# Kernel tuning notes

Measured on AMD Instinct MI355X. Metric: run time of the kernel, lower is better.

## Reference

```python
import jax, jax.numpy as jnp
import numpy as np

L = 768          # temporal feature length
C_IN = 2048      # feature channels
NA = 10          # anchor scales per position
NC = 21          # num classes (20 + bg)
PRE_NMS = 1024   # pre-NMS top-k
POST_NMS = 128   # fixed proposal count after NMS
NMS_THR = 0.7
SCALE = 1.0      # cfg.Process.new_dilation*new_cluster/Frame
ANCHOR_SIZES = np.array([2., 4., 5., 6., 8., 9., 10., 12., 14., 16.], np.float32)


def _conv(x, w, b, pad=0):
    # x: [N,C,T], w: [O,I,K]
    y = jax.lax.conv_general_dilated(x, w, (1,), [(pad, pad)],
                                     dimension_numbers=('NCH', 'OIH', 'NCH'))
    return y + b[None, :, None]


def _lin(x, w, b):
    return x @ w.T + b


def _forward(feature, p):
    f = _conv(feature, p['w1f'], p['b1f'], 1)
    f = _conv(f, p['w2f'], p['b2f'], 1)
    x = _conv(f, p['wc1'], p['bc1'], 0)                      # [1,512,L]
    # SegmentProposal tower (relu only after conv4, as in source)
    h = _conv(x, p['sp1w'], p['sp1b'], 1)
    h = _conv(h, p['sp2w'], p['sp2b'], 1)
    h = _conv(h, p['sp3w'], p['sp3b'], 1)
    h = jax.nn.relu(_conv(h, p['sp4w'], p['sp4b'], 1))
    cls_score = _conv(h, p['spcw'], p['spcb'], 0)            # [1,2*NA,L]
    seg_pred = _conv(h, p['spsw'], p['spsb'], 0)             # [1,2*NA,L]

    def _resh(t):  # [1,2NA,L] -> [L*NA,2]  (transpose(2,1).view(B,L,C/2,2))
        return jnp.transpose(t, (0, 2, 1)).reshape(-1, 2)

    cls2 = _resh(cls_score)
    cls_prob = jax.nn.softmax(cls2, -1)
    off2 = _resh(seg_pred)

    # anchors: (center, half_len) per position per scale, position-major
    centers = (jnp.arange(L, dtype=jnp.float32) + 0.5) * SCALE
    halves = jnp.asarray(ANCHOR_SIZES) * 0.5
    a_c = jnp.repeat(centers, NA)
    a_h = jnp.tile(halves, L)
    im_info = L * SCALE

    # apply offsets: center shift + log-length scale, clip to video extent
    c = a_c + off2[:, 0] * (2.0 * a_h)
    hl = a_h * jnp.exp(off2[:, 1])
    s = jnp.clip(c - hl, 0.0, im_info)
    e = jnp.clip(c + hl, 0.0, im_info)
    scores = cls_prob[:, 1]

    top_sc, top_i = jax.lax.top_k(scores, PRE_NMS)
    ss, ee = s[top_i], e[top_i]

    def body(i, keep):
        inter = jnp.maximum(0., jnp.minimum(ee, ee[i]) - jnp.maximum(ss, ss[i]))
        union = (ee - ss) + (ee[i] - ss[i]) - inter
        iou = inter / jnp.maximum(union, 1e-8)
        sup = (iou > NMS_THR) & (jnp.arange(PRE_NMS) > i) & keep[i]
        return keep & ~sup

    keep = jax.lax.fori_loop(0, PRE_NMS, body, jnp.ones(PRE_NMS, bool))
    order = jnp.argsort((~keep).astype(jnp.int32), stable=True)  # kept first, score order
    sel = order[:POST_NMS]
    pidx = top_i[sel]
    ps, pe = s[pidx], e[pidx]
    pbbox = jnp.stack([(ps + pe) * 0.5, (pe - ps) * 0.5], -1)    # (center, half)

    # map proposals to feature index range (floor/ceil + clamp, as in source)
    st = jnp.clip(jnp.floor((pbbox[:, 0] - pbbox[:, 1]) / SCALE), 0, L - 1).astype(jnp.int32)
    en = jnp.clip(jnp.ceil((pbbox[:, 0] + pbbox[:, 1]) / SCALE), 0, L - 1).astype(jnp.int32)
    en = jnp.maximum(en, st)

    feat = f[0]                                              # [C_IN, L]
    tpos = jnp.arange(L)
    bins = jnp.arange(7)

    def roi_pool(se):  # AdaptiveMaxPool1d(7) over feat[:, s0:e0+1]
        s0, e0 = se
        ln = e0 - s0 + 1
        bs = s0 + (bins * ln) // 7
        be = s0 + ((bins + 1) * ln + 6) // 7 - 1
        m = (tpos[None, :] >= bs[:, None]) & (tpos[None, :] <= be[:, None])  # [7,L]
        v = jnp.where(m[None], feat[:, None, :], -jnp.inf)   # [C_IN,7,L]
        return v.max(-1)                                     # [C_IN,7]

    spp = jax.lax.map(roi_pool, (st, en))                    # [K,C_IN,7]

    y = _conv(spp, p['wc2'], p['bc2'], 0)
    y = _conv(y, p['w3'], p['b3'], 1)
    y = jax.nn.relu(_conv(y, p['w4'], p['b4'], 1))
    y = _conv(y, p['w5'], p['b5'], 1)
    y = jax.nn.relu(_conv(y, p['w6'], p['b6'], 1))
    y = y.reshape(y.shape[0], -1)                            # [K, 512*7]
    y = _lin(y, p['fc1w'], p['fc1b'])
    # Relation attention is computed but unused in the source forward -> omitted
    y = jax.nn.relu(y)
    y = _lin(y, p['fc2w'], p['fc2b'])
    y = _lin(y, p['fc3w'], p['fc3b'])
    obj_cls = _lin(y, p['clsw'], p['clsb'])                  # [K,NC]
    obj_off = _lin(y, p['boxw'], p['boxb']).reshape(-1, NC - 1, 2)
    cls_sel = cls2[pidx]                                     # [K,2]
    off_sel = off2[pidx]                                     # [K,2]
    return cls_sel, off_sel, obj_cls, obj_off


_PARAM_SHAPES = {
    'w1f': (2048, 2048, 3), 'b1f': (2048,),
    'w2f': (2048, 2048, 3), 'b2f': (2048,),
    'wc1': (512, 2048, 1), 'bc1': (512,),
    'sp1w': (512, 512, 3), 'sp1b': (512,),
    'sp2w': (512, 512, 3), 'sp2b': (512,),
    'sp3w': (512, 512, 3), 'sp3b': (512,),
    'sp4w': (512, 512, 3), 'sp4b': (512,),
    'spcw': (2 * NA, 512, 1), 'spcb': (2 * NA,),
    'spsw': (2 * NA, 512, 1), 'spsb': (2 * NA,),
    'wc2': (512, 2048, 1), 'bc2': (512,),
    'w3': (512, 512, 3), 'b3': (512,),
    'w4': (512, 512, 3), 'b4': (512,),
    'w5': (512, 512, 3), 'b5': (512,),
    'w6': (512, 512, 3), 'b6': (512,),
    'fc1w': (512, 512 * 7), 'fc1b': (512,),
    'fc2w': (256, 512), 'fc2b': (256,),
    'fc3w': (128, 256), 'fc3b': (128,),
    'clsw': (NC, 128), 'clsb': (NC,),
    'boxw': (2 * (NC - 1), 128), 'boxb': (2 * (NC - 1),),
}


def setup_inputs() -> dict:
    key = jax.random.key(0)
    inp = {'feature': jax.random.normal(jax.random.fold_in(key, 0), (1, C_IN, L), jnp.float32)}
    for i, (name, shp) in enumerate(sorted(_PARAM_SHAPES.items())):
        k = jax.random.fold_in(key, i + 1)
        inp[name] = jax.random.normal(k, shp, jnp.float32) * 0.02
    return inp


def reference(feature, b1f, b2f, b3, b4, b5, b6, bc1, bc2, boxb, boxw, clsb, clsw,
              fc1b, fc1w, fc2b, fc2w, fc3b, fc3w, sp1b, sp1w, sp2b, sp2w, sp3b, sp3w,
              sp4b, sp4w, spcb, spcw, spsb, spsw, w1f, w2f, w3, w4, w5, w6,
              wc1, wc2):
    p = dict(w1f=w1f, b1f=b1f, w2f=w2f, b2f=b2f, wc1=wc1, bc1=bc1,
             sp1w=sp1w, sp1b=sp1b, sp2w=sp2w, sp2b=sp2b, sp3w=sp3w, sp3b=sp3b,
             sp4w=sp4w, sp4b=sp4b, spcw=spcw, spcb=spcb, spsw=spsw, spsb=spsb,
             wc2=wc2, bc2=bc2, w3=w3, b3=b3, w4=w4, b4=b4, w5=w5, b5=b5,
             w6=w6, b6=b6, fc1w=fc1w, fc1b=fc1b, fc2w=fc2w, fc2b=fc2b,
             fc3w=fc3w, fc3b=fc3b, clsw=clsw, clsb=clsb, boxw=boxw, boxb=boxb)
    return _forward(feature, p)
```

## Files before the change

### kernel.cpp

```cpp
#include <hip/hip_runtime.h>

typedef __attribute__((ext_vector_type(8))) short short8;
typedef __attribute__((ext_vector_type(4))) float float4v;

__device__ __forceinline__ float bf(unsigned short u) {
    return __uint_as_float(((unsigned int)u) << 16);
}
__device__ __forceinline__ unsigned short f2b(float f) {
    unsigned int u = __float_as_uint(f);
    unsigned int r = (u + 0x7FFFu + ((u >> 16) & 1u)) >> 16;
    return (unsigned short)r;
}

__constant__ float c_anchors[10] = {2.f,4.f,5.f,6.f,8.f,9.f,10.f,12.f,14.f,16.f};

__global__ __launch_bounds__(256) void zeroXt_kernel(unsigned short* __restrict__ Xt, int CI) {
    int i = blockIdx.x * 256 + threadIdx.x;
    if (i < 2 * CI) {
        int row = (i >= CI) ? 769 : 0;
        int co = (i >= CI) ? (i - CI) : i;
        Xt[(size_t)row * CI + co] = 0;
        Xt[(size_t)770 * CI + (size_t)row * CI + co] = 0;
    }
}

__global__ __launch_bounds__(256) void decomp_kernel(const float* __restrict__ src,
                                                     unsigned short* __restrict__ Xt, int CI) {
    __shared__ float T[32][33];
    int l0 = blockIdx.x * 32, ci0 = blockIdx.y * 32;
    int tid = threadIdx.x;
#pragma unroll
    for (int i = 0; i < 4; i++) {
        int slot = tid + 256 * i;
        int r = slot >> 5, c = slot & 31;
        T[r][c] = src[(size_t)(ci0 + r) * 768 + l0 + c];
    }
    __syncthreads();
    unsigned short* Xh = Xt;
    unsigned short* Xl = Xt + (size_t)770 * CI;
#pragma unroll
    for (int i = 0; i < 4; i++) {
        int slot = tid + 256 * i;
        int li = slot >> 5, cc = slot & 31;
        float v = T[cc][li];
        unsigned short h = f2b(v);
        float lo = v - bf(h);
        size_t o = (size_t)(l0 + li + 1) * CI + ci0 + cc;
        Xh[o] = h;
        Xl[o] = f2b(lo);
    }
}

template <int TAPS>
__global__ __launch_bounds__(512, 6) void convmm_kernel(const float* __restrict__ W,
                                                        const unsigned short* __restrict__ Xt,
                                                        float* __restrict__ G,
                                                        int CO, int CI, int S) {
    constexpr int RS = TAPS * 32 + 8;
    __shared__ unsigned short At[2][64 * RS];
    __shared__ unsigned short Bt[2][130 * 40];
    int tid = threadIdx.x;
    int lane = tid & 63, wid = tid >> 6;
    int q = lane >> 4, ln = lane & 15;
    int co0 = blockIdx.x * 64;
    int l0 = blockIdx.y * 128;
    int s = blockIdx.z;
    int kPer = CI / S, cis = s * kPer;
    const unsigned short* Xh = Xt;
    const unsigned short* Xl = Xt + (size_t)770 * CI;

    float4v zero4 = {0.f, 0.f, 0.f, 0.f};
    float4v acc[2][2];
    acc[0][0] = zero4; acc[0][1] = zero4; acc[1][0] = zero4; acc[1][1] = zero4;

    int wave_m = (wid >> 2) * 32;
    int wave_n = (wid & 3) * 32;

    for (int kb = 0; kb < kPer; kb += 32) {
        int cib = cis + kb;
        if (TAPS == 3) {
#pragma unroll
            for (int i = 0; i < 2; i++) {
                int slot = tid + 512 * i;
                int row = slot >> 4, ci0 = (slot & 15) * 2;
                const float* wp = W + ((size_t)(co0 + row) * CI + cib + ci0) * 3;
                float fa[6];
#pragma unroll
                for (int j = 0; j < 6; j++) fa[j] = wp[j];
#pragma unroll
                for (int t = 0; t < 3; t++) {
                    unsigned short h0 = f2b(fa[t]);
                    unsigned short h1 = f2b(fa[t + 3]);
                    unsigned short e0 = f2b(fa[t] - bf(h0));
                    unsigned short e1 = f2b(fa[t + 3] - bf(h1));
                    *(unsigned int*)&At[0][row * RS + t * 32 + ci0] =
                        (unsigned int)h0 | ((unsigned int)h1 << 16);
                    *(unsigned int*)&At[1][row * RS + t * 32 + ci0] =
                        (unsigned int)e0 | ((unsigned int)e1 << 16);
                }
            }
        } else {
            int row = tid >> 3, ci0 = (tid & 7) * 4;
            float4 wv = *(const float4*)(W + (size_t)(co0 + row) * CI + cib + ci0);
            float fa[4] = {wv.x, wv.y, wv.z, wv.w};
            unsigned short h[4], e[4];
#pragma unroll
            for (int j = 0; j < 4; j++) {
                h[j] = f2b(fa[j]);
                e[j] = f2b(fa[j] - bf(h[j]));
            }
            unsigned long long hp = (unsigned long long)h[0] | ((unsigned long long)h[1] << 16) |
                                    ((unsigned long long)h[2] << 32) | ((unsigned long long)h[3] << 48);
            unsigned long long ep = (unsigned long long)e[0] | ((unsigned long long)e[1] << 16) |
                                    ((unsigned long long)e[2] << 32) | ((unsigned long long)e[3] << 48);
            *(unsigned long long*)&At[0][row * RS + ci0] = hp;
            *(unsigned long long*)&At[1][row * RS + ci0] = ep;
        }
#pragma unroll
        for (int i = 0; i < 3; i++) {
            int slot = tid + 512 * i;
            if (slot < 1040) {
                int p = slot >= 520 ? 1 : 0;
                int rem = slot - p * 520;
                int r = rem >> 2, qq = rem & 3;
                const unsigned short* src = (p ? Xl : Xh) + (size_t)(l0 + r) * CI + cib + qq * 8;
                short8 v = *(const short8*)src;
                *(short8*)&Bt[p][r * 40 + qq * 8] = v;
            }
        }
        __syncthreads();
#pragma unroll
        for (int t = 0; t < TAPS; t++) {
            int shift = (TAPS == 1) ? 1 : t;
            short8 bh[2], bl[2];
#pragma unroll
            for (int nf = 0; nf < 2; nf++) {
                int rrow = wave_n + nf * 16 + ln + shift;
                bh[nf] = *(const short8*)&Bt[0][rrow * 40 + q * 8];
                bl[nf] = *(const short8*)&Bt[1][rrow * 40 + q * 8];
            }
#pragma unroll
            for (int mf = 0; mf < 2; mf++) {
                int mrow = wave_m + mf * 16 + ln;
                short8 ah = *(const short8*)&At[0][mrow * RS + t * 32 + q * 8];
                short8 al = *(const short8*)&At[1][mrow * RS + t * 32 + q * 8];
#pragma unroll
                for (int nf = 0; nf < 2; nf++) {
                    acc[mf][nf] = __builtin_amdgcn_mfma_f32_16x16x32_bf16(ah, bh[nf], acc[mf][nf], 0, 0, 0);
                    acc[mf][nf] = __builtin_amdgcn_mfma_f32_16x16x32_bf16(ah, bl[nf], acc[mf][nf], 0, 0, 0);
                    acc[mf][nf] = __builtin_amdgcn_mfma_f32_16x16x32_bf16(al, bh[nf], acc[mf][nf], 0, 0, 0);
                }
            }
        }
        __syncthreads();
    }
    float* Gz = G + (size_t)s * CO * 768;
#pragma unroll
    for (int mf = 0; mf < 2; mf++)
#pragma unroll
        for (int nf = 0; nf < 2; nf++) {
            int col = l0 + wave_n + nf * 16 + ln;
            int rowb = co0 + wave_m + mf * 16 + q * 4;
#pragma unroll
            for (int r = 0; r < 4; r++)
                Gz[(size_t)(rowb + r) * 768 + col] = acc[mf][nf][r];
        }
}

__global__ __launch_bounds__(256) void finsum_x_kernel(const float* __restrict__ G,
                                                       const float* __restrict__ bias,
                                                       unsigned short* __restrict__ Xt,
                                                       int CO, int P) {
    __shared__ float T[64][65];
    int co0 = blockIdx.x * 64, l0 = blockIdx.y * 64;
    int tid = threadIdx.x;
#pragma unroll 1
    for (int i = 0; i < 16; i++) {
        int slot = tid + 256 * i;
        int r = slot >> 6, c = slot & 63;
        float v = bias[co0 + r];
        for (int p = 0; p < P; p++) v += G[((size_t)p * CO + co0 + r) * 768 + l0 + c];
        T[r][c] = v;
    }
    __syncthreads();
    unsigned short* Xh = Xt;
    unsigned short* Xl = Xt + (size_t)770 * CO;
#pragma unroll 1
    for (int i = 0; i < 16; i++) {
        int slot = tid + 256 * i;
        int li = slot >> 6, ci = slot & 63;
        float v = T[ci][li];
        unsigned short h = f2b(v);
        float lo = v - bf(h);
        size_t o = (size_t)(l0 + li + 1) * CO + co0 + ci;
        Xh[o] = h;
        Xl[o] = f2b(lo);
    }
}

__global__ __launch_bounds__(256) void finsum_xf_kernel(const float* __restrict__ G,
                                                        const float* __restrict__ bias,
                                                        unsigned short* __restrict__ Xt,
                                                        float* __restrict__ outF,
                                                        int CO, int P) {
    __shared__ float T[64][65];
    int co0 = blockIdx.x * 64, l0 = blockIdx.y * 64;
    int tid = threadIdx.x;
#pragma unroll 1
    for (int i = 0; i < 16; i++) {
        int slot = tid + 256 * i;
        int r = slot >> 6, c = slot & 63;
        float v = bias[co0 + r];
        for (int p = 0; p < P; p++) v += G[((size_t)p * CO + co0 + r) * 768 + l0 + c];
        T[r][c] = v;
        outF[(size_t)(co0 + r) * 768 + l0 + c] = v;
    }
    __syncthreads();
    unsigned short* Xh = Xt;
    unsigned short* Xl = Xt + (size_t)770 * CO;
#pragma unroll 1
    for (int i = 0; i < 16; i++) {
        int slot = tid + 256 * i;
        int li = slot >> 6, ci = slot & 63;
        float v = T[ci][li];
        unsigned short h = f2b(v);
        float lo = v - bf(h);
        size_t o = (size_t)(l0 + li + 1) * CO + co0 + ci;
        Xh[o] = h;
        Xl[o] = f2b(lo);
    }
}

__global__ __launch_bounds__(256) void finsum_f_kernel(const float* __restrict__ G,
                                                       const float* __restrict__ bias,
                                                       float* __restrict__ out,
                                                       int CO, int P, int relu) {
    int i = blockIdx.x * 256 + threadIdx.x;
    if (i >= CO * 768) return;
    int r = i / 768, c = i - r * 768;
    float v = bias[r];
    for (int p = 0; p < P; p++) v += G[((size_t)p * CO + r) * 768 + c];
    if (relu) v = fmaxf(v, 0.f);
    out[i] = v;
}

__global__ __launch_bounds__(256) void finalize_kernel(const float* __restrict__ part,
                                                       float* __restrict__ out,
                                                       const float* __restrict__ bias,
                                                       int RPAD, int R, int NCOLS, int S, int relu) {
    int i = blockIdx.x * 256 + threadIdx.x;
    int total = R * NCOLS;
    if (i >= total) return;
    int r = i / NCOLS;
    int c = i - r * NCOLS;
    float v = 0.f;
    for (int s = 0; s < S; s++) v += part[((size_t)s * RPAD + r) * NCOLS + c];
    v += bias[r];
    if (relu) v = fmaxf(v, 0.f);
    out[i] = v;
}

template <int MODE, int EPI>
__global__ __launch_bounds__(256) void gemm_kernel(const float* __restrict__ W,
                                                   const float* __restrict__ B,
                                                   const float* __restrict__ bias,
                                                   float* __restrict__ outF,
                                                   int R, int K, int NCOLS, int LDB, int S, int relu) {
    __shared__ __align__(16) float Bt[16][68];
    __shared__ __align__(16) float Wt[16][68];
    int tid = threadIdx.x;
    int tx = tid & 15, ty = tid >> 4;
    int r0 = blockIdx.x * 64, c0 = blockIdx.y * 64, s = blockIdx.z;
    int kPer = K / S;
    int k0s = s * kPer;
    float acc[4][4] = {};
    for (int kb = 0; kb < kPer; kb += 16) {
        int k0 = k0s + kb;
        {
            int rr = r0 + (tid >> 2);
            int q = tid & 3;
            float4 wv4 = {0.f, 0.f, 0.f, 0.f};
            if (rr < R) wv4 = *(const float4*)(W + (size_t)rr * K + k0 + q * 4);
            Wt[q * 4 + 0][tid >> 2] = wv4.x;
            Wt[q * 4 + 1][tid >> 2] = wv4.y;
            Wt[q * 4 + 2][tid >> 2] = wv4.z;
            Wt[q * 4 + 3][tid >> 2] = wv4.w;
        }
#pragma unroll
        for (int p = 0; p < 4; p++) {
            int kk = p * 4 + (tid >> 6);
            int c = tid & 63;
            int k = k0 + kk;
            int col = c0 + c;
            float v;
            if (MODE == 0) {
                v = B[(size_t)k * LDB + col];
            } else if (MODE == 1) {
                int ci = k / 3;
                int t = k - ci * 3;
                int lc = (col % 7) + t - 1;
                v = ((unsigned)lc < 7u) ? B[(size_t)ci * 896 + col + t - 1] : 0.f;
            } else {
                int co = k / 7;
                int b7 = k - co * 7;
                v = B[(size_t)co * 896 + col * 7 + b7];
            }
            Bt[kk][c] = v;
        }
        __syncthreads();
#pragma unroll
        for (int kk = 0; kk < 16; kk++) {
            float4 bv = *(const float4*)&Bt[kk][tx * 4];
            float4 wv = *(const float4*)&Wt[kk][ty * 4];
            float bb[4] = {bv.x, bv.y, bv.z, bv.w};
            float ww[4] = {wv.x, wv.y, wv.z, wv.w};
#pragma unroll
            for (int i = 0; i < 4; i++)
#pragma unroll
                for (int j = 0; j < 4; j++)
                    acc[i][j] = fmaf(ww[i], bb[j], acc[i][j]);
        }
        __syncthreads();
    }
    if (EPI == 0) {
        if (S > 1) {
#pragma unroll
            for (int i = 0; i < 4; i++) {
                int r = r0 + ty * 4 + i;
                float4 o = {acc[i][0], acc[i][1], acc[i][2], acc[i][3]};
                *(float4*)&outF[((size_t)s * R + r) * NCOLS + c0 + tx * 4] = o;
            }
        } else {
#pragma unroll
            for (int i = 0; i < 4; i++) {
                int r = r0 + ty * 4 + i;
                if (r < R) {
                    float bv = bias[r];
#pragma unroll
                    for (int j = 0; j < 4; j++) {
                        float v = acc[i][j] + bv;
                        if (relu) v = fmaxf(v, 0.f);
                        outF[(size_t)r * NCOLS + c0 + tx * 4 + j] = v;
                    }
                }
            }
        }
    } else {
#pragma unroll
        for (int i = 0; i < 4; i++) {
            int r = r0 + ty * 4 + i;
            if (r < R) {
                float bv = bias[r];
#pragma unroll
                for (int j = 0; j < 4; j++) {
                    int col = c0 + tx * 4 + j;
                    float v = acc[i][j] + bv;
                    if (EPI == 1) outF[512 + col * 21 + r] = v;
                    else outF[3200 + col * 40 + r] = v;
                }
            }
        }
    }
}

__global__ __launch_bounds__(256) void proposal_kernel(const float* __restrict__ clsS,
                                                       const float* __restrict__ segS,
                                                       float* __restrict__ cls2, float* __restrict__ off2,
                                                       float* __restrict__ scores,
                                                       float* __restrict__ sArr, float* __restrict__ eArr) {
    int i = blockIdx.x * 256 + threadIdx.x;
    if (i >= 7680) return;
    int l = i / 10;
    int a = i - l * 10;
    float c0 = clsS[(a * 2 + 0) * 768 + l];
    float c1 = clsS[(a * 2 + 1) * 768 + l];
    cls2[i * 2] = c0;
    cls2[i * 2 + 1] = c1;
    float m = fmaxf(c0, c1);
    float e0 = expf(c0 - m), e1 = expf(c1 - m);
    scores[i] = e1 / (e0 + e1);
    float o0 = segS[(a * 2 + 0) * 768 + l];
    float o1 = segS[(a * 2 + 1) * 768 + l];
    off2[i * 2] = o0;
    off2[i * 2 + 1] = o1;
    float ah = c_anchors[a] * 0.5f;
    float ac = (float)l + 0.5f;
    float c = ac + o0 * (2.f * ah);
    float hl = ah * expf(o1);
    sArr[i] = fminf(fmaxf(c - hl, 0.f), 768.f);
    eArr[i] = fminf(fmaxf(c + hl, 0.f), 768.f);
}

__global__ __launch_bounds__(1024) void sort_kernel(const float* __restrict__ scores,
                                                    const float* __restrict__ sArr, const float* __restrict__ eArr,
                                                    int* __restrict__ topI,
                                                    float* __restrict__ ss, float* __restrict__ ee) {
    __shared__ unsigned long long kk[8192];
    int tid = threadIdx.x;
#pragma unroll
    for (int m = 0; m < 8; m++) {
        int i = tid + m * 1024;
        unsigned long long key = 0ull;
        if (i < 7680) {
            unsigned int sb = __float_as_uint(scores[i]);
            key = ((unsigned long long)sb << 32) | (unsigned long long)(0xFFFFFFFFu - (unsigned)i);
        }
        kk[i] = key;
    }
    __syncthreads();
    for (int k = 2; k <= 8192; k <<= 1) {
        for (int j = k >> 1; j > 0; j >>= 1) {
#pragma unroll 1
            for (int m = 0; m < 8; m++) {
                int i = tid + m * 1024;
                int ixj = i ^ j;
                if (ixj > i) {
                    unsigned long long a = kk[i], b = kk[ixj];
                    bool descend = ((i & k) == 0);
                    if (descend ? (a < b) : (a > b)) { kk[i] = b; kk[ixj] = a; }
                }
            }
            __syncthreads();
        }
    }
    int idx = (int)(0xFFFFFFFFu - (unsigned int)(kk[tid] & 0xFFFFFFFFull));
    topI[tid] = idx;
    ss[tid] = sArr[idx];
    ee[tid] = eArr[idx];
}

__global__ __launch_bounds__(256) void nms_mask_kernel(const float* __restrict__ ss, const float* __restrict__ ee,
                                                       unsigned long long* __restrict__ mask) {
    int g = blockIdx.x * 256 + threadIdx.x;
    int i = g >> 4, w = g & 15;
    float si = ss[i], ei = ee[i];
    unsigned long long bits = 0ull;
#pragma unroll 1
    for (int jj = 0; jj < 64; jj++) {
        int j = w * 64 + jj;
        if (j > i) {
            float sj = ss[j], ej = ee[j];
            float inter = fmaxf(0.f, fminf(ei, ej) - fmaxf(si, sj));
            float uni = (ej - sj) + (ei - si) - inter;
            float iou = inter / fmaxf(uni, 1e-8f);
            if (iou > 0.7f) bits |= (1ull << jj);
        }
    }
    mask[(size_t)i * 16 + w] = bits;
}

__global__ __launch_bounds__(64) void nms_select_kernel(const unsigned long long* __restrict__ mask,
                                                        const int* __restrict__ topI,
                                                        const float* __restrict__ ss, const float* __restrict__ ee,
                                                        const float* __restrict__ cls2, const float* __restrict__ off2,
                                                        int* __restrict__ stA, int* __restrict__ enA,
                                                        float* __restrict__ out) {
    __shared__ unsigned long long remvS[16];
    __shared__ unsigned long long keepS[16];
    __shared__ int prefixS[17];
    int lane = threadIdx.x;
    if (lane < 16) remvS[lane] = 0ull;
    __syncthreads();
#pragma unroll 1
    for (int b = 0; b < 16; b++) {
        int row = b * 64 + lane;
        const unsigned long long* mrow = mask + (size_t)row * 16;
        unsigned long long diag = mrow[b];
        unsigned long long later[15];
        int nlater = 15 - b;
#pragma unroll 1
        for (int c = 0; c < nlater; c++) later[c] = mrow[b + 1 + c];
        unsigned long long rem = remvS[b];
#pragma unroll 1
        for (int i = 0; i < 64; i++) {
            unsigned long long di = __shfl(diag, i);
            if (!((rem >> i) & 1ull)) rem |= di;
        }
        unsigned long long keep64 = ~rem;
        bool mykeep = (keep64 >> lane) & 1ull;
#pragma unroll 1
        for (int c = 0; c < nlater; c++) {
            unsigned long long v = mykeep ? later[c] : 0ull;
            for (int sft = 1; sft < 64; sft <<= 1) v |= __shfl_xor(v, sft);
            if (lane == 0) remvS[b + 1 + c] |= v;
        }
        if (lane == 0) keepS[b] = keep64;
        __syncthreads();
    }
    if (lane == 0) {
        int acc = 0;
        for (int b = 0; b < 16; b++) { prefixS[b] = acc; acc += __popcll(keepS[b]); }
        prefixS[16] = acc;
    }
    __syncthreads();
    int total = prefixS[16];
#pragma unroll 1
    for (int b = 0; b < 16; b++) {
        int tid = b * 64 + lane;
        unsigned long long keep64 = keepS[b];
        unsigned long long below = (lane == 0) ? 0ull : (keep64 << (64 - lane));
        int keptBefore = prefixS[b] + __popcll(below);
        int kp = (int)((keep64 >> lane) & 1ull);
        int pos = kp ? keptBefore : (total + tid - keptBefore);
        if (pos < 128) {
            int orig = topI[tid];
            float ps = ss[tid], pe = ee[tid];
            out[pos * 2 + 0] = cls2[orig * 2 + 0];
            out[pos * 2 + 1] = cls2[orig * 2 + 1];
            out[256 + pos * 2 + 0] = off2[orig * 2 + 0];
            out[256 + pos * 2 + 1] = off2[orig * 2 + 1];
            float bc = (ps + pe) * 0.5f, bh = (pe - ps) * 0.5f;
            int st = (int)fminf(fmaxf(floorf(bc - bh), 0.f), 767.f);
            int en = (int)fminf(fmaxf(ceilf(bc + bh), 0.f), 767.f);
            if (en < st) en = st;
            stA[pos] = st;
            enA[pos] = en;
        }
    }
}

__global__ __launch_bounds__(256) void roi_kernel(const float* __restrict__ f,
                                                  const int* __restrict__ stA, const int* __restrict__ enA,
                                                  float* __restrict__ spp) {
    int n = blockIdx.x;
    int c = blockIdx.y * 256 + threadIdx.x;
    int st = stA[n], en = enA[n];
    int ln = en - st + 1;
    const float* row = f + (size_t)c * 768;
#pragma unroll 1
    for (int b = 0; b < 7; b++) {
        int bs = st + (b * ln) / 7;
        int be = st + ((b + 1) * ln + 6) / 7 - 1;
        float m = row[bs];
        for (int t = bs + 1; t <= be; t++) m = fmaxf(m, row[t]);
        spp[(size_t)c * 896 + n * 7 + b] = m;
    }
}

extern "C" void kernel_launch(void* const* d_in, const int* in_sizes, int n_in,
                              void* d_out, int out_size, void* d_ws, size_t ws_size,
                              hipStream_t stream) {
    const float* IN[39];
    for (int i = 0; i < 39; i++) IN[i] = (const float*)d_in[i];
    const float* feature = IN[0];
    const float *b1f = IN[1], *b2f = IN[2], *b3 = IN[3], *b4 = IN[4], *b5 = IN[5], *b6 = IN[6];
    const float *bc1 = IN[7], *bc2 = IN[8], *boxb = IN[9], *boxw = IN[10];
    const float *clsb = IN[11], *clsw = IN[12];
    const float *fc1b = IN[13], *fc1w = IN[14], *fc2b = IN[15], *fc2w = IN[16];
    const float *fc3b = IN[17], *fc3w = IN[18];
    const float *sp1b = IN[19], *sp1w = IN[20], *sp2b = IN[21], *sp2w = IN[22];
    const float *sp3b = IN[23], *sp3w = IN[24], *sp4b = IN[25], *sp4w = IN[26];
    const float *spcb = IN[27], *spcw = IN[28], *spsb = IN[29], *spsw = IN[30];
    const float *w1f = IN[31], *w2f = IN[32], *w3w = IN[33], *w4w = IN[34];
    const float *w5w = IN[35], *w6w = IN[36], *wc1 = IN[37], *wc2 = IN[38];
    float* out = (float*)d_out;

    char* base = (char*)d_ws;
    float* G    = (float*)base;
    float* part = (float*)base;
    float* spp  = (float*)(base + 14680064);
    float* yA   = (float*)(base + 22020096);
    float* yB   = (float*)(base + 23855104);
    float* g1   = (float*)(base + 25690112);
    float* g2   = (float*)(base + 25952256);
    float* g3   = (float*)(base + 26083328);
    size_t off = 26148864;
    auto alloc = [&](size_t bytes) { void* p = base + off; off += (bytes + 15) & ~((size_t)15); return p; };
    unsigned short* Xt = (unsigned short*)alloc((size_t)770 * 2048 * 2 * 2);
    float* fbuf = (float*)alloc((size_t)2048 * 768 * 4);
    float* hB   = (float*)alloc((size_t)512 * 768 * 4);
    float* clsS = (float*)alloc((size_t)20 * 768 * 4);
    float* segS = (float*)alloc((size_t)20 * 768 * 4);
    float* cls2 = (float*)alloc(7680 * 2 * 4);
    float* off2 = (float*)alloc(7680 * 2 * 4);
    float* scores = (float*)alloc(7680 * 4);
    float* sArr = (float*)alloc(7680 * 4);
    float* eArr = (float*)alloc(7680 * 4);
    float* ssS  = (float*)alloc(1024 * 4);
    float* eeS  = (float*)alloc(1024 * 4);
    unsigned long long* mask = (unsigned long long*)alloc((size_t)16384 * 8);
    int* topI = (int*)alloc(1024 * 4);
    int* stA = (int*)alloc(128 * 4);
    int* enA = (int*)alloc(128 * 4);

    dim3 blk(256);
    dim3 blk512(512);

    zeroXt_kernel<<<16, blk, 0, stream>>>(Xt, 2048);
    decomp_kernel<<<dim3(24, 64), blk, 0, stream>>>(feature, Xt, 2048);
    convmm_kernel<3><<<dim3(32, 6, 4), blk512, 0, stream>>>(w1f, Xt, G, 2048, 2048, 4);
    finsum_x_kernel<<<dim3(32, 12), blk, 0, stream>>>(G, b1f, Xt, 2048, 4);
    convmm_kernel<3><<<dim3(32, 6, 4), blk512, 0, stream>>>(w2f, Xt, G, 2048, 2048, 4);
    finsum_xf_kernel<<<dim3(32, 12), blk, 0, stream>>>(G, b2f, Xt, fbuf, 2048, 4);

    convmm_kernel<1><<<dim3(8, 6, 8), blk512, 0, stream>>>(wc1, Xt, G, 512, 2048, 8);
    zeroXt_kernel<<<4, blk, 0, stream>>>(Xt, 512);
    finsum_x_kernel<<<dim3(8, 12), blk, 0, stream>>>(G, bc1, Xt, 512, 8);

    convmm_kernel<3><<<dim3(8, 6, 8), blk512, 0, stream>>>(sp1w, Xt, G, 512, 512, 8);
    finsum_x_kernel<<<dim3(8, 12), blk, 0, stream>>>(G, sp1b, Xt, 512, 8);
    convmm_kernel<3><<<dim3(8, 6, 8), blk512, 0, stream>>>(sp2w, Xt, G, 512, 512, 8);
    finsum_x_kernel<<<dim3(8, 12), blk, 0, stream>>>(G, sp2b, Xt, 512, 8);
    convmm_kernel<3><<<dim3(8, 6, 8), blk512, 0, stream>>>(sp3w, Xt, G, 512, 512, 8);
    finsum_x_kernel<<<dim3(8, 12), blk, 0, stream>>>(G, sp3b, Xt, 512, 8);
    convmm_kernel<3><<<dim3(8, 6, 8), blk512, 0, stream>>>(sp4w, Xt, G, 512, 512, 8);
    finsum_f_kernel<<<1536, blk, 0, stream>>>(G, sp4b, hB, 512, 8, 1);

    gemm_kernel<0, 0><<<dim3(1, 12, 1), blk, 0, stream>>>(spcw, hB, spcb, clsS, 20, 512, 768, 768, 1, 0);
    gemm_kernel<0, 0><<<dim3(1, 12, 1), blk, 0, stream>>>(spsw, hB, spsb, segS, 20, 512, 768, 768, 1, 0);

    proposal_kernel<<<30, blk, 0, stream>>>(clsS, segS, cls2, off2, scores, sArr, eArr);
    sort_kernel<<<1, 1024, 0, stream>>>(scores, sArr, eArr, topI, ssS, eeS);
    nms_mask_kernel<<<64, blk, 0, stream>>>(ssS, eeS, mask);
    nms_select_kernel<<<1, 64, 0, stream>>>(mask, topI, ssS, eeS, cls2, off2, stA, enA, out);

    roi_kernel<<<dim3(128, 8), blk, 0, stream>>>(fbuf, stA, enA, spp);

    gemm_kernel<0, 0><<<dim3(8, 14, 8), blk, 0, stream>>>(wc2, spp, bc2, part, 512, 2048, 896, 896, 8, 0);
    finalize_kernel<<<1792, blk, 0, stream>>>(part, yA, bc2, 512, 512, 896, 8, 0);

    gemm_kernel<1, 0><<<dim3(8, 14, 8), blk, 0, stream>>>(w3w, yA, b3, part, 512, 1536, 896, 896, 8, 0);
    finalize_kernel<<<1792, blk, 0, stream>>>(part, yB, b3, 512, 512, 896, 8, 0);
    gemm_kernel<1, 0><<<dim3(8, 14, 8), blk, 0, stream>>>(w4w, yB, b4, part, 512, 1536, 896, 896, 8, 0);
    finalize_kernel<<<1792, blk, 0, stream>>>(part, yA, b4, 512, 512, 896, 8, 1);
    gemm_kernel<1, 0><<<dim3(8, 14, 8), blk, 0, stream>>>(w5w, yA, b5, part, 512, 1536, 896, 896, 8, 0);
    finalize_kernel<<<1792, blk, 0, stream>>>(part, yB, b5, 512, 512, 896, 8, 0);
    gemm_kernel<1, 0><<<dim3(8, 14, 8), blk, 0, stream>>>(w6w, yB, b6, part, 512, 1536, 896, 896, 8, 0);
    finalize_kernel<<<1792, blk, 0, stream>>>(part, yA, b6, 512, 512, 896, 8, 1);

    gemm_kernel<2, 0><<<dim3(8, 2, 28), blk, 0, stream>>>(fc1w, yA, fc1b, part, 512, 3584, 128, 128, 28, 0);
    finalize_kernel<<<256, blk, 0, stream>>>(part, g1, fc1b, 512, 512, 128, 28, 1);

    gemm_kernel<0, 0><<<dim3(4, 2, 4), blk, 0, stream>>>(fc2w, g1, fc2b, part, 256, 512, 128, 128, 4, 0);
    finalize_kernel<<<128, blk, 0, stream>>>(part, g2, fc2b, 256, 256, 128, 4, 0);
    gemm_kernel<0, 0><<<dim3(2, 2, 2), blk, 0, stream>>>(fc3w, g2, fc3b, part, 128, 256, 128, 128, 2, 0);
    finalize_kernel<<<64, blk, 0, stream>>>(part, g3, fc3b, 128, 128, 128, 2, 0);

    gemm_kernel<0, 1><<<dim3(1, 2, 1), blk, 0, stream>>>(clsw, g3, clsb, out, 21, 128, 128, 128, 1, 0);
    gemm_kernel<0, 2><<<dim3(1, 2, 1), blk, 0, stream>>>(boxw, g3, boxb, out, 40, 128, 128, 128, 1, 0);
}
```

Before: 1.207 ms.

## Split top-k sort into parallel block sorts plus top-1024 merge tree

```diff
diff --git a/kernel.cpp b/kernel.cpp
--- a/kernel.cpp
+++ b/kernel.cpp
@@ -391,39 +391,66 @@
     eArr[i] = fminf(fmaxf(c + hl, 0.f), 768.f);
 }
 
-__global__ __launch_bounds__(1024) void sort_kernel(const float* __restrict__ scores,
-                                                    const float* __restrict__ sArr, const float* __restrict__ eArr,
-                                                    int* __restrict__ topI,
-                                                    float* __restrict__ ss, float* __restrict__ ee) {
-    __shared__ unsigned long long kk[8192];
+__global__ __launch_bounds__(1024) void sortA_kernel(const float* __restrict__ scores,
+                                                     unsigned long long* __restrict__ runs) {
+    __shared__ unsigned long long kk[1024];
     int tid = threadIdx.x;
-#pragma unroll
-    for (int m = 0; m < 8; m++) {
-        int i = tid + m * 1024;
-        unsigned long long key = 0ull;
-        if (i < 7680) {
-            unsigned int sb = __float_as_uint(scores[i]);
-            key = ((unsigned long long)sb << 32) | (unsigned long long)(0xFFFFFFFFu - (unsigned)i);
-        }
-        kk[i] = key;
-    }
+    int gbase = blockIdx.x * 1024;
+    int gi = gbase + tid;
+    unsigned long long key = 0ull;
+    if (gi < 7680) {
+        unsigned int sb = __float_as_uint(scores[gi]);
+        key = ((unsigned long long)sb << 32) | (unsigned long long)(0xFFFFFFFFu - (unsigned)gi);
+    }
+    kk[tid] = key;
     __syncthreads();
-    for (int k = 2; k <= 8192; k <<= 1) {
+    for (int k = 2; k <= 1024; k <<= 1) {
         for (int j = k >> 1; j > 0; j >>= 1) {
-#pragma unroll 1
-            for (int m = 0; m < 8; m++) {
-                int i = tid + m * 1024;
-                int ixj = i ^ j;
-                if (ixj > i) {
-                    unsigned long long a = kk[i], b = kk[ixj];
-                    bool descend = ((i & k) == 0);
-                    if (descend ? (a < b) : (a > b)) { kk[i] = b; kk[ixj] = a; }
+            int ixj = tid ^ j;
+            if (ixj > tid) {
+                unsigned long long a = kk[tid], b = kk[ixj];
+                bool descend = ((tid & k) == 0);
+                if (descend ? (a < b) : (a > b)) { kk[tid] = b; kk[ixj] = a; }
+            }
+            __syncthreads();
+        }
+    }
+    runs[gbase + tid] = kk[tid];
+}
+
+__global__ __launch_bounds__(1024) void sortB_kernel(const unsigned long long* __restrict__ runs,
+                                                     const float* __restrict__ sArr, const float* __restrict__ eArr,
+                                                     int* __restrict__ topI,
+                                                     float* __restrict__ ss, float* __restrict__ ee) {
+    __shared__ unsigned long long S[8192];
+    int tid = threadIdx.x;
+#pragma unroll
+    for (int m = 0; m < 8; m++) S[m * 1024 + tid] = runs[m * 1024 + tid];
+    __syncthreads();
+#pragma unroll 1
+    for (int level = 0; level < 3; level++) {
+        int span = 1024 << level;
+        int nm = 4 >> level;
+        for (int m = 0; m < nm; m++) {
+            int baseA = m * (span * 2);
+            int baseB = baseA + span;
+            unsigned long long a = S[baseA + tid], b = S[baseB + 1023 - tid];
+            S[baseA + tid] = (a > b) ? a : b;
+        }
+        __syncthreads();
+        for (int j = 512; j > 0; j >>= 1) {
+            for (int m = 0; m < nm; m++) {
+                int baseA = m * (span * 2);
+                int ixj = tid ^ j;
+                if (ixj > tid) {
+                    unsigned long long a = S[baseA + tid], b = S[baseA + ixj];
+                    if (a < b) { S[baseA + tid] = b; S[baseA + ixj] = a; }
                 }
             }
             __syncthreads();
         }
     }
-    int idx = (int)(0xFFFFFFFFu - (unsigned int)(kk[tid] & 0xFFFFFFFFull));
+    int idx = (int)(0xFFFFFFFFu - (unsigned int)(S[tid] & 0xFFFFFFFFull));
     topI[tid] = idx;
     ss[tid] = sArr[idx];
     ee[tid] = eArr[idx];
@@ -578,6 +605,7 @@
     float* eArr = (float*)alloc(7680 * 4);
     float* ssS  = (float*)alloc(1024 * 4);
     float* eeS  = (float*)alloc(1024 * 4);
+    unsigned long long* runs = (unsigned long long*)alloc((size_t)8192 * 8);
     unsigned long long* mask = (unsigned long long*)alloc((size_t)16384 * 8);
     int* topI = (int*)alloc(1024 * 4);
     int* stA = (int*)alloc(128 * 4);
@@ -610,7 +638,8 @@
     gemm_kernel<0, 0><<<dim3(1, 12, 1), blk, 0, stream>>>(spsw, hB, spsb, segS, 20, 512, 768, 768, 1, 0);
 
     proposal_kernel<<<30, blk, 0, stream>>>(clsS, segS, cls2, off2, scores, sArr, eArr);
-    sort_kernel<<<1, 1024, 0, stream>>>(scores, sArr, eArr, topI, ssS, eeS);
+    sortA_kernel<<<8, 1024, 0, stream>>>(scores, runs);
+    sortB_kernel<<<1, 1024, 0, stream>>>(runs, sArr, eArr, topI, ssS, eeS);
     nms_mask_kernel<<<64, blk, 0, stream>>>(ssS, eeS, mask);
     nms_select_kernel<<<1, 64, 0, stream>>>(mask, topI, ssS, eeS, cls2, off2, stA, enA, out);
 
```

Measured after the change: 1.111 ms. -7.9%, faster.
